# Kernel optimization log

Hardware: AMD Instinct MI355X
Metric: run time of the kernel (lower is better)

The kernel has to match this reference:

```python
import jax, jax.numpy as jnp
import numpy as np

J, C, F, K = 4096, 8192, 64, 2  # jobs, total nodes, out feats, TAGConv hops (DGL default K=2)


def setup_inputs() -> dict:
    key = jax.random.key(0)
    ks = jax.random.split(key, 8)
    h = jax.random.uniform(ks[0], (J,), jnp.float32)
    L = jax.random.uniform(ks[1], (J,), jnp.float32)
    W = jax.random.uniform(ks[2], (), jnp.float32)
    P = jax.random.uniform(ks[3], (), jnp.float32)
    N = jax.random.uniform(ks[4], (), jnp.float32)
    Graph = jax.random.randint(ks[5], (J, C), 0, 2).astype(jnp.float32)
    tag_w = jax.random.normal(ks[6], ((K + 1) * 6, F), jnp.float32) * 0.05  # TAGConv lin weight on concat of K+1 hops
    tag_b = jnp.zeros((F,), jnp.float32)
    lin_w = jax.random.normal(ks[7], (F, C), jnp.float32) * 0.05
    lin_b = jnp.zeros((C,), jnp.float32)
    return dict(h=h, L=L, W=W, P=P, N=N, Graph=Graph,
                tag_w=tag_w, tag_b=tag_b, lin_w=lin_w, lin_b=lin_b)


def _mask(Graph):
    Jn, Cn = Graph.shape
    row = Graph.sum(axis=1, keepdims=True)          # [J,1]
    col = Graph.sum(axis=0, keepdims=True)          # [1,C]
    colJ = col[:, :Jn]                               # [1,J]
    left = 1.0 - row - row.T - colJ - colJ.T         # [J,J]
    left = jnp.where(left == 1.0, 1.0, 0.0)
    left = jnp.triu(left, k=1)
    right = 1.0 - jnp.broadcast_to(row, (Jn, Cn - Jn))
    return jnp.concatenate([left, right], axis=1)    # [J,C]


def reference(h, L, W, P, N, Graph, tag_w, tag_b, lin_w, lin_b):
    Jn, Cn = Graph.shape
    # sort jobs by h descending, pair with L
    order = jnp.argsort(-h)
    jobList = jnp.stack([h[order], L[order]], axis=1)                 # [J,2]
    other = jnp.stack([W, P, N, jnp.asarray(1.0, h.dtype)])           # [4]
    X = jnp.concatenate([jobList, jnp.broadcast_to(other, (Jn, 4))], axis=1)  # [J,6]
    X = jnp.concatenate([X, jnp.zeros((Cn - Jn, 6), X.dtype)], axis=0)        # [C,6]
    # pad adjacency to square CxC
    A = jnp.concatenate([Graph, jnp.zeros((Cn - Jn, Cn), Graph.dtype)], axis=0)
    # DGL TAGConv: norm = clamp(in_deg,1)^-0.5; edge i->j iff A[i,j]==1 => aggregate = A^T @ x
    deg = A.sum(axis=0)
    norm = jnp.clip(deg, 1.0) ** -0.5

    def prop(x):
        return (A.T @ (x * norm[:, None])) * norm[:, None]

    f0 = X
    f1 = prop(f0)
    f2 = prop(f1)
    G_t = jnp.concatenate([f0, f1, f2], axis=1) @ tag_w + tag_b       # [C,F]
    Value = G_t[:Jn] @ lin_w + lin_b                                   # [J,C]
    tmp = Value - (1.0 - _mask(Graph)) * 10000.0
    Poss = jax.nn.softmax(tmp.reshape(-1)).reshape(tmp.shape)
    return (Value, Poss)
```

## Files before the change

kernel.cpp:

```cpp
#include <hip/hip_runtime.h>
#include <math.h>

#define JN 4096
#define CN 8192

typedef __attribute__((ext_vector_type(8))) short short8;
typedef __attribute__((ext_vector_type(4))) short short4v;
typedef __attribute__((ext_vector_type(4))) float f32x4;

#define WS_LWT    0
#define WS_GTB    262144
#define WS_ROWSUM 393216
#define WS_DEG    397312
#define WS_NORM   401408
#define WS_X      405504
#define WS_F1     430080
#define WS_PART   454656

#define PS_BITR    0
#define PS_P1      524288
#define PS_P2      917504

__device__ __forceinline__ unsigned short f2bf(float x) {
    unsigned int u = __float_as_uint(x);
    u += 0x7fffu + ((u >> 16) & 1u);
    return (unsigned short)(u >> 16);
}

__device__ __forceinline__ float gt_val(const float* __restrict__ x, const float* __restrict__ a,
                                        const float* __restrict__ b, const float* __restrict__ tw,
                                        float acc, int f) {
#pragma unroll
    for (int k = 0; k < 6; ++k) acc += x[k] * tw[k * 64 + f];
#pragma unroll
    for (int k = 0; k < 6; ++k) acc += a[k] * tw[(k + 6) * 64 + f];
#pragma unroll
    for (int k = 0; k < 6; ++k) acc += b[k] * tw[(k + 12) * 64 + f];
    return acc;
}

__global__ __launch_bounds__(256) void k_front(const float* __restrict__ G,
                                               const float* __restrict__ h, const float* __restrict__ L,
                                               const float* __restrict__ Wp, const float* __restrict__ Pp,
                                               const float* __restrict__ Np,
                                               const float* __restrict__ lw,
                                               float* __restrict__ rowsum,
                                               unsigned long long* __restrict__ bitR,
                                               float* __restrict__ X,
                                               unsigned short* __restrict__ lwT,
                                               float* __restrict__ deg) {
    __shared__ float redf[4];
    __shared__ int redi[4];
    __shared__ float s_t[64][65];
    int wv = threadIdx.x >> 6, lane = threadIdx.x & 63;
    if (blockIdx.x < JN) {
        int row = blockIdx.x;
        const f32x4* g4 = (const f32x4*)(G + (size_t)row * CN);
        unsigned long long* brow = bitR + (size_t)row * 64;
        float s = 0.f;
#pragma unroll
        for (int i = 0; i < 4; ++i) {
            f32x4 v = __builtin_nontemporal_load(&g4[i * 256 + wv * 64 + lane]);
            s += v[0] + v[1] + v[2] + v[3];
            unsigned long long b0 = __ballot(v[0] != 0.f);
            unsigned long long b1 = __ballot(v[1] != 0.f);
            unsigned long long b2 = __ballot(v[2] != 0.f);
            unsigned long long b3 = __ballot(v[3] != 0.f);
            if (!lane) {
                int base = i * 16 + wv * 4;
                brow[base] = b0; brow[base + 1] = b1; brow[base + 2] = b2; brow[base + 3] = b3;
            }
        }
#pragma unroll
        for (int i = 4; i < 8; ++i) {
            f32x4 v = __builtin_nontemporal_load(&g4[i * 256 + wv * 64 + lane]);
            s += v[0] + v[1] + v[2] + v[3];
        }
        for (int o = 32; o; o >>= 1) s += __shfl_down(s, o, 64);
        if (!lane) redf[wv] = s;
        __syncthreads();
        if (!threadIdx.x) rowsum[row] = redf[0] + redf[1] + redf[2] + redf[3];
    } else if (blockIdx.x < 2 * JN) {
        int i = blockIdx.x - JN;
        float hi = h[i];
        int cnt = 0;
        for (int j = threadIdx.x; j < JN; j += 256) {
            float hj = h[j];
            cnt += (hj > hi) || (hj == hi && j < i);
        }
        for (int o = 32; o; o >>= 1) cnt += __shfl_down(cnt, o, 64);
        if (!lane) redi[wv] = cnt;
        __syncthreads();
        if (!threadIdx.x) {
            int r = redi[0] + redi[1] + redi[2] + redi[3];
            float* xr = X + r * 6;
            xr[0] = hi; xr[1] = L[i]; xr[2] = *Wp; xr[3] = *Pp; xr[4] = *Np; xr[5] = 1.f;
        }
    } else if (blockIdx.x < 2 * JN + 128) {
        int c0 = (blockIdx.x - 2 * JN) * 64;
        for (int t = threadIdx.x; t < 4096; t += 256) {
            int f = t >> 6, cc = t & 63;
            s_t[f][cc] = lw[(size_t)f * CN + c0 + cc];
        }
        __syncthreads();
        for (int q = threadIdx.x; q < 512; q += 256) {
            int c = q >> 3, kc = q & 7;
            short8 pack;
#pragma unroll
            for (int i = 0; i < 8; ++i) pack[i] = (short)f2bf(s_t[kc * 8 + i][c]);
            *(short8*)(lwT + ((size_t)(c0 + c)) * 64 + kc * 8) = pack;
        }
    } else {
        for (int t = threadIdx.x; t < JN; t += 256) deg[t] = 0.f;
    }
}

__global__ __launch_bounds__(256) void k_colsum_bits(const unsigned long long* __restrict__ bitR,
                                                     float* __restrict__ deg) {
    __shared__ unsigned long long s_bits[256][4];
    int bx = blockIdx.x, r0 = blockIdx.y * 256;
    int tid = threadIdx.x;
    for (int t = tid; t < 1024; t += 256) {
        int r = t >> 2, wl = t & 3;
        s_bits[r][wl] = bitR[(size_t)(r0 + r) * 64 + bx * 4 + wl];
    }
    __syncthreads();
    int wl = tid & 3, bit = tid >> 2;
    int cnt = 0;
    for (int r = 0; r < 256; ++r)
        cnt += (int)((s_bits[r][wl] >> bit) & 1ull);
    atomicAdd(&deg[bx * 256 + tid], (float)cnt);
}

__global__ __launch_bounds__(256) void k_prop1(const unsigned long long* __restrict__ bitR,
                                               const float* __restrict__ X,
                                               const float* __restrict__ deg,
                                               float* __restrict__ norm,
                                               float* __restrict__ part) {
    __shared__ unsigned long long s_bits[256][4];
    __shared__ float s_in[1536];
    __shared__ float s_norm[256];
    int bx = blockIdx.x, r0 = blockIdx.y * 256;
    int tid = threadIdx.x;
    {
        float d = deg[r0 + tid];
        float dc = d < 1.f ? 1.f : d;
        float nv = rsqrtf(dc);
        s_norm[tid] = nv;
        if (bx == 0) norm[r0 + tid] = nv;
    }
    for (int t = tid; t < 1024; t += 256) {
        int r = t >> 2, wl = t & 3;
        s_bits[r][wl] = bitR[(size_t)(r0 + r) * 64 + bx * 4 + wl];
    }
    __syncthreads();
    for (int t = tid; t < 1536; t += 256)
        s_in[t] = X[r0 * 6 + t] * s_norm[t / 6];
    __syncthreads();
    int wl = tid & 3, bit = tid >> 2;
    float a0 = 0, a1 = 0, a2 = 0, a3 = 0, a4 = 0, a5 = 0;
    for (int r = 0; r < 256; ++r) {
        float g = (float)((s_bits[r][wl] >> bit) & 1ull);
        const float* x = &s_in[r * 6];
        a0 += g * x[0]; a1 += g * x[1]; a2 += g * x[2];
        a3 += g * x[3]; a4 += g * x[4]; a5 += g * x[5];
    }
    float* o = part + ((size_t)blockIdx.y * JN + bx * 256 + tid) * 6;
    o[0] = a0; o[1] = a1; o[2] = a2; o[3] = a3; o[4] = a4; o[5] = a5;
}

__global__ __launch_bounds__(256) void k_prop2(const unsigned long long* __restrict__ bitR,
                                               const float* __restrict__ p1, const float* __restrict__ norm,
                                               float* __restrict__ f1, float* __restrict__ part) {
    __shared__ unsigned long long s_bits[256][4];
    __shared__ float s_in[1536];
    int bx = blockIdx.x, r0 = blockIdx.y * 256;
    int tid = threadIdx.x;
    for (int t = tid; t < 1024; t += 256) {
        int r = t >> 2, wl = t & 3;
        s_bits[r][wl] = bitR[(size_t)(r0 + r) * 64 + bx * 4 + wl];
    }
    for (int t = tid; t < 1536; t += 256) {
        float s = 0.f;
        for (int ch = 0; ch < 16; ++ch) s += p1[(size_t)ch * 24576 + r0 * 6 + t];
        int row = r0 + t / 6;
        float n = norm[row];
        float f1v = s * n;
        if (bx == 0) f1[r0 * 6 + t] = f1v;
        s_in[t] = f1v * n;
    }
    __syncthreads();
    int wl = tid & 3, bit = tid >> 2;
    float a0 = 0, a1 = 0, a2 = 0, a3 = 0, a4 = 0, a5 = 0;
    for (int r = 0; r < 256; ++r) {
        float g = (float)((s_bits[r][wl] >> bit) & 1ull);
        const float* x = &s_in[r * 6];
        a0 += g * x[0]; a1 += g * x[1]; a2 += g * x[2];
        a3 += g * x[3]; a4 += g * x[4]; a5 += g * x[5];
    }
    float* o = part + ((size_t)blockIdx.y * JN + bx * 256 + tid) * 6;
    o[0] = a0; o[1] = a1; o[2] = a2; o[3] = a3; o[4] = a4; o[5] = a5;
}

__global__ __launch_bounds__(256) void k_gt(const float* __restrict__ p2, const float* __restrict__ norm,
                                            const float* __restrict__ f1, const float* __restrict__ X,
                                            const float* __restrict__ tw, const float* __restrict__ tb,
                                            unsigned short* __restrict__ Gtb) {
    __shared__ float s_x[64 * 6], s_f1[64 * 6], s_f2[64 * 6];
    __shared__ float s_tw[18 * 64], s_tb[64];
    int j0 = blockIdx.x * 64, tid = threadIdx.x;
    for (int t = tid; t < 1152; t += 256) s_tw[t] = tw[t];
    if (tid < 64) s_tb[tid] = tb[tid];
    for (int t = tid; t < 384; t += 256) {
        s_x[t] = X[j0 * 6 + t];
        s_f1[t] = f1[j0 * 6 + t];
        float s = 0.f;
        for (int ch = 0; ch < 16; ++ch) s += p2[(size_t)ch * 24576 + j0 * 6 + t];
        s_f2[t] = s * norm[j0 + t / 6];
    }
    __syncthreads();
    int row = tid & 63, fg = tid >> 6;
    float xv[6], av[6], bv[6];
#pragma unroll
    for (int k = 0; k < 6; ++k) {
        xv[k] = s_x[row * 6 + k]; av[k] = s_f1[row * 6 + k]; bv[k] = s_f2[row * 6 + k];
    }
    short8 p0, p1v;
#pragma unroll
    for (int i = 0; i < 16; ++i) {
        int f = fg * 16 + i;
        float acc = gt_val(xv, av, bv, s_tw, s_tb[f], f);
        unsigned short u = f2bf(acc);
        if (i < 8) p0[i] = (short)u; else p1v[i - 8] = (short)u;
    }
    *(short8*)(Gtb + (size_t)(j0 + row) * 64 + fg * 16) = p0;
    *(short8*)(Gtb + (size_t)(j0 + row) * 64 + fg * 16 + 8) = p1v;
}

#define GEMM_DECLS()                                                                      \
    __shared__ unsigned short sGt[64 * 64];                                               \
    __shared__ unsigned short sW[256 * 64];                                               \
    float* sRedM = (float*)sGt;                                                           \
    float* sRedS = ((float*)sGt) + 4;                                                     \
    float* sG    = ((float*)sGt) + 8;                                                     \
    (void)sRedM; (void)sRedS; (void)sG;

#define GEMM_BODY()                                                                       \
    int j0 = blockIdx.y * 64, c0 = blockIdx.x * 256, tid = threadIdx.x;                   \
    for (int q = tid; q < 2048; q += 256) {                                               \
        int col = q >> 3, off = q & 7;                                                    \
        short8 v = *(const short8*)(lwT + ((size_t)(c0 + col)) * 64 + off * 8);           \
        int byte = (col * 128 + off * 16) ^ ((col & 7) << 4);                             \
        *(short8*)((char*)sW + byte) = v;                                                 \
    }                                                                                     \
    for (int q = tid; q < 512; q += 256) {                                                \
        int row = q >> 3, off = q & 7;                                                    \
        short8 v = *(const short8*)(Gtb + ((size_t)(j0 + row)) * 64 + off * 8);           \
        int byte = (row * 128 + off * 16) ^ ((row & 7) << 4);                             \
        *(short8*)((char*)sGt + byte) = v;                                                \
    }                                                                                     \
    __syncthreads();                                                                      \
    int lane = tid & 63, w = tid >> 6;                                                    \
    int lrow = lane & 15, kg = lane >> 4;                                                 \
    f32x4 acc[4][4];                                            \
    for (int m = 0; m < 4; ++m)                                                           \
        for (int n = 0; n < 4; ++n) acc[m][n] = (f32x4){0.f, 0.f, 0.f, 0.f};              \
    for (int ks = 0; ks < 2; ++ks) {                                                      \
        int kb = ks * 64 + kg * 16;                                                       \
        short8 wf[4], gf[4];                                                              \
        for (int m = 0; m < 4; ++m) {                                                     \
            int col = w * 64 + m * 16 + lrow;                                             \
            wf[m] = *(const short8*)((const char*)sW + ((col * 128 + kb) ^ ((col & 7) << 4))); \
        }                                                                                 \
        for (int n = 0; n < 4; ++n) {                                                     \
            int row = n * 16 + lrow;                                                      \
            gf[n] = *(const short8*)((const char*)sGt + ((row * 128 + kb) ^ ((row & 7) << 4))); \
        }                                                                                 \
        for (int m = 0; m < 4; ++m)                                                       \
            for (int n = 0; n < 4; ++n)                                                   \
                acc[m][n] = __builtin_amdgcn_mfma_f32_16x16x32_bf16(wf[m], gf[n], acc[m][n], 0, 0, 0); \
    }                                                                                     \
    __syncthreads();                 \
    bool left = (c0 < JN);                                                                \
    int cb[4]; f32x4 lb4[4], rsc4[4], dgc4[4];                                            \
    for (int m = 0; m < 4; ++m) {                                                         \
        cb[m] = c0 + w * 64 + m * 16 + kg * 4;                                            \
        lb4[m] = *(const f32x4*)&lb[cb[m]];                                               \
        if (left) { rsc4[m] = *(const f32x4*)&rowsum[cb[m]]; dgc4[m] = *(const f32x4*)&deg[cb[m]]; } \
        else      { rsc4[m] = (f32x4){0,0,0,0}; dgc4[m] = (f32x4){0,0,0,0}; }             \
    }

__global__ __launch_bounds__(256) void k_valueA(const unsigned short* __restrict__ Gtb,
                                                const unsigned short* __restrict__ lwT,
                                                const float* __restrict__ lb,
                                                const float* __restrict__ rowsum, const float* __restrict__ deg,
                                                float* __restrict__ Value, float* __restrict__ partials) {
    GEMM_DECLS()
    GEMM_BODY()

    float mx = -INFINITY;
#pragma unroll
    for (int n = 0; n < 4; ++n) {
        int j = j0 + n * 16 + lrow;
        float rs_i = rowsum[j], dg_i = deg[j];
#pragma unroll
        for (int m = 0; m < 4; ++m) {
            f32x4 v4 = acc[m][n] + lb4[m];
            __builtin_nontemporal_store(v4, (f32x4*)&Value[(size_t)j * CN + cb[m]]);
            f32x4 t4;
#pragma unroll
            for (int u = 0; u < 4; ++u) {
                float om;
                if (left) {
                    bool m1 = ((rs_i + rsc4[m][u] + dg_i + dgc4[m][u]) == 0.0f) && (cb[m] + u > j);
                    om = m1 ? 0.f : 1.f;
                } else {
                    om = rs_i;
                }
                t4[u] = v4[u] - om * 10000.f;
            }
            acc[m][n] = t4;
            mx = fmaxf(fmaxf(fmaxf(mx, t4[0]), t4[1]), fmaxf(t4[2], t4[3]));
        }
    }
    float sm = 0.f;
#pragma unroll
    for (int n = 0; n < 4; ++n)
#pragma unroll
        for (int m = 0; m < 4; ++m)
#pragma unroll
            for (int u = 0; u < 4; ++u) sm += __expf(acc[m][n][u] - mx);

    for (int o = 32; o; o >>= 1) {
        float om_ = __shfl_down(mx, o, 64);
        float os_ = __shfl_down(sm, o, 64);
        float nm = fmaxf(mx, om_);
        sm = sm * __expf(mx - nm) + os_ * __expf(om_ - nm);
        mx = nm;
    }
    if (!lane) { sRedM[w] = mx; sRedS[w] = sm; }
    __syncthreads();
    if (!tid) {
        float M = sRedM[0], S = sRedS[0];
        for (int i = 1; i < 4; ++i) {
            float nm = fmaxf(M, sRedM[i]);
            S = S * __expf(M - nm) + sRedS[i] * __expf(sRedM[i] - nm);
            M = nm;
        }
        int bid = blockIdx.y * gridDim.x + blockIdx.x;
        partials[2 * bid] = M;
        partials[2 * bid + 1] = S;
    }
}

__global__ __launch_bounds__(256) void k_valueB(const unsigned short* __restrict__ Gtb,
                                                const unsigned short* __restrict__ lwT,
                                                const float* __restrict__ lb,
                                                const float* __restrict__ rowsum, const float* __restrict__ deg,
                                                const float* __restrict__ partials, float* __restrict__ Poss) {
    GEMM_DECLS()
    {
        int tid0 = threadIdx.x;
        float mx = -INFINITY, sm = 0.f;
        for (int i = tid0; i < 2048; i += 256) {
            float m = partials[2 * i], s = partials[2 * i + 1];
            float nm = fmaxf(mx, m);
            sm = sm * __expf(mx - nm) + s * __expf(m - nm);
            mx = nm;
        }
        for (int o = 32; o; o >>= 1) {
            float om_ = __shfl_down(mx, o, 64);
            float os_ = __shfl_down(sm, o, 64);
            float nm = fmaxf(mx, om_);
            sm = sm * __expf(mx - nm) + os_ * __expf(om_ - nm);
            mx = nm;
        }
        int lane0 = tid0 & 63, w0 = tid0 >> 6;
        if (!lane0) { sRedM[w0] = mx; sRedS[w0] = sm; }
        __syncthreads();
        if (!tid0) {
            float M = sRedM[0], S = sRedS[0];
            for (int i = 1; i < 4; ++i) {
                float nm = fmaxf(M, sRedM[i]);
                S = S * __expf(M - nm) + sRedS[i] * __expf(sRedM[i] - nm);
                M = nm;
            }
            sG[0] = M; sG[1] = S;
        }
        __syncthreads();
    }
    float gmax = sG[0];
    float ginv = 1.0f / sG[1];
    __syncthreads();

    GEMM_BODY()
#pragma unroll
    for (int n = 0; n < 4; ++n) {
        int j = j0 + n * 16 + lrow;
        float rs_i = rowsum[j], dg_i = deg[j];
#pragma unroll
        for (int m = 0; m < 4; ++m) {
            f32x4 v4 = acc[m][n] + lb4[m];
            f32x4 o4;
#pragma unroll
            for (int u = 0; u < 4; ++u) {
                float om;
                if (left) {
                    bool m1 = ((rs_i + rsc4[m][u] + dg_i + dgc4[m][u]) == 0.0f) && (cb[m] + u > j);
                    om = m1 ? 0.f : 1.f;
                } else {
                    om = rs_i;
                }
                o4[u] = __expf(v4[u] - om * 10000.f - gmax) * ginv;
            }
            __builtin_nontemporal_store(o4, (f32x4*)&Poss[(size_t)j * CN + cb[m]]);
        }
    }
}

extern "C" void kernel_launch(void* const* d_in, const int* in_sizes, int n_in,
                              void* d_out, int out_size, void* d_ws, size_t ws_size,
                              hipStream_t stream) {
    const float* h  = (const float*)d_in[0];
    const float* L  = (const float*)d_in[1];
    const float* W  = (const float*)d_in[2];
    const float* P  = (const float*)d_in[3];
    const float* N  = (const float*)d_in[4];
    const float* G  = (const float*)d_in[5];
    const float* tw = (const float*)d_in[6];
    const float* tb = (const float*)d_in[7];
    const float* lw = (const float*)d_in[8];
    const float* lb = (const float*)d_in[9];

    float* ws = (float*)d_ws;
    unsigned short* lwT = (unsigned short*)(ws + WS_LWT);
    unsigned short* Gtb = (unsigned short*)(ws + WS_GTB);
    float* rowsum = ws + WS_ROWSUM;
    float* deg    = ws + WS_DEG;
    float* norm   = ws + WS_NORM;
    float* X      = ws + WS_X;
    float* f1     = ws + WS_F1;
    float* part   = ws + WS_PART;

    float* Value = (float*)d_out;
    float* Poss  = Value + (size_t)JN * CN;

    unsigned long long* bitR = (unsigned long long*)(Poss + PS_BITR);
    float* p1      = Poss + PS_P1;
    float* p2      = Poss + PS_P2;

    k_front      <<<2 * JN + 129, 256, 0, stream>>>(G, h, L, W, P, N, lw, rowsum, bitR, X, lwT, deg);
    k_colsum_bits<<<dim3(16, 16), 256, 0, stream>>>(bitR, deg);
    k_prop1      <<<dim3(16, 16), 256, 0, stream>>>(bitR, X, deg, norm, p1);
    k_prop2      <<<dim3(16, 16), 256, 0, stream>>>(bitR, p1, norm, f1, p2);
    k_gt         <<<64, 256, 0, stream>>>(p2, norm, f1, X, tw, tb, Gtb);
    k_valueA     <<<dim3(32, 64), 256, 0, stream>>>(Gtb, lwT, lb, rowsum, deg, Value, part);
    k_valueB     <<<dim3(32, 64), 256, 0, stream>>>(Gtb, lwT, lb, rowsum, deg, part, Poss);
}
```

Measured before the change: 149.5 us.

## Fuse G_t computation into value GEMM kernels and merge front blocks

Removes the separate k_gt kernel: each value-GEMM block now recomputes its 64-row G_t tile from X, f1 and f2 straight into shared memory, and k_valueA saves f2 to workspace for k_valueB. The rank-sort work is also folded into the row-sum blocks of k_front, so its grid is halved. This saves one launch and a Gtb round trip through global memory. The cost is redundant G_t computation across the 32 column blocks, plus an extra 16-chunk p2 reduction in every k_valueA block.

```diff
diff --git a/kernel.cpp b/kernel.cpp
--- a/kernel.cpp
+++ b/kernel.cpp
@@ -5,11 +5,10 @@
 #define CN 8192
 
 typedef __attribute__((ext_vector_type(8))) short short8;
-typedef __attribute__((ext_vector_type(4))) short short4v;
 typedef __attribute__((ext_vector_type(4))) float f32x4;
 
 #define WS_LWT    0
-#define WS_GTB    262144
+#define WS_F2     262144
 #define WS_ROWSUM 393216
 #define WS_DEG    397312
 #define WS_NORM   401408
@@ -80,13 +79,12 @@
         if (!lane) redf[wv] = s;
         __syncthreads();
         if (!threadIdx.x) rowsum[row] = redf[0] + redf[1] + redf[2] + redf[3];
-    } else if (blockIdx.x < 2 * JN) {
-        int i = blockIdx.x - JN;
-        float hi = h[i];
+
+        float hi = h[row];
         int cnt = 0;
         for (int j = threadIdx.x; j < JN; j += 256) {
             float hj = h[j];
-            cnt += (hj > hi) || (hj == hi && j < i);
+            cnt += (hj > hi) || (hj == hi && j < row);
         }
         for (int o = 32; o; o >>= 1) cnt += __shfl_down(cnt, o, 64);
         if (!lane) redi[wv] = cnt;
@@ -94,10 +92,10 @@
         if (!threadIdx.x) {
             int r = redi[0] + redi[1] + redi[2] + redi[3];
             float* xr = X + r * 6;
-            xr[0] = hi; xr[1] = L[i]; xr[2] = *Wp; xr[3] = *Pp; xr[4] = *Np; xr[5] = 1.f;
-        }
-    } else if (blockIdx.x < 2 * JN + 128) {
-        int c0 = (blockIdx.x - 2 * JN) * 64;
+            xr[0] = hi; xr[1] = L[row]; xr[2] = *Wp; xr[3] = *Pp; xr[4] = *Np; xr[5] = 1.f;
+        }
+    } else if (blockIdx.x < JN + 128) {
+        int c0 = (blockIdx.x - JN) * 64;
         for (int t = threadIdx.x; t < 4096; t += 256) {
             int f = t >> 6, cc = t & 63;
             s_t[f][cc] = lw[(size_t)f * CN + c0 + cc];
@@ -202,62 +200,52 @@
     o[0] = a0; o[1] = a1; o[2] = a2; o[3] = a3; o[4] = a4; o[5] = a5;
 }
 
-__global__ __launch_bounds__(256) void k_gt(const float* __restrict__ p2, const float* __restrict__ norm,
-                                            const float* __restrict__ f1, const float* __restrict__ X,
-                                            const float* __restrict__ tw, const float* __restrict__ tb,
-                                            unsigned short* __restrict__ Gtb) {
-    __shared__ float s_x[64 * 6], s_f1[64 * 6], s_f2[64 * 6];
-    __shared__ float s_tw[18 * 64], s_tb[64];
-    int j0 = blockIdx.x * 64, tid = threadIdx.x;
-    for (int t = tid; t < 1152; t += 256) s_tw[t] = tw[t];
-    if (tid < 64) s_tb[tid] = tb[tid];
-    for (int t = tid; t < 384; t += 256) {
-        s_x[t] = X[j0 * 6 + t];
-        s_f1[t] = f1[j0 * 6 + t];
-        float s = 0.f;
-        for (int ch = 0; ch < 16; ++ch) s += p2[(size_t)ch * 24576 + j0 * 6 + t];
-        s_f2[t] = s * norm[j0 + t / 6];
-    }
-    __syncthreads();
-    int row = tid & 63, fg = tid >> 6;
-    float xv[6], av[6], bv[6];
-#pragma unroll
-    for (int k = 0; k < 6; ++k) {
-        xv[k] = s_x[row * 6 + k]; av[k] = s_f1[row * 6 + k]; bv[k] = s_f2[row * 6 + k];
-    }
-    short8 p0, p1v;
-#pragma unroll
-    for (int i = 0; i < 16; ++i) {
-        int f = fg * 16 + i;
-        float acc = gt_val(xv, av, bv, s_tw, s_tb[f], f);
-        unsigned short u = f2bf(acc);
-        if (i < 8) p0[i] = (short)u; else p1v[i - 8] = (short)u;
-    }
-    *(short8*)(Gtb + (size_t)(j0 + row) * 64 + fg * 16) = p0;
-    *(short8*)(Gtb + (size_t)(j0 + row) * 64 + fg * 16 + 8) = p1v;
-}
-
 #define GEMM_DECLS()                                                                      \
     __shared__ unsigned short sGt[64 * 64];                                               \
     __shared__ unsigned short sW[256 * 64];                                               \
     float* sRedM = (float*)sGt;                                                           \
     float* sRedS = ((float*)sGt) + 4;                                                     \
     float* sG    = ((float*)sGt) + 8;                                                     \
+    float* s_tw  = (float*)sW;                                                            \
+    float* s_tb  = ((float*)sW) + 1152;                                                   \
+    float* s_x   = ((float*)sW) + 1216;                                                   \
+    float* s_a   = ((float*)sW) + 1600;                                                   \
+    float* s_b   = ((float*)sW) + 1984;                                                   \
     (void)sRedM; (void)sRedS; (void)sG;
 
-#define GEMM_BODY()                                                                       \
+#define GEMM_BODY(F2_INIT)                                                                \
     int j0 = blockIdx.y * 64, c0 = blockIdx.x * 256, tid = threadIdx.x;                   \
-    for (int q = tid; q < 2048; q += 256) {                                               \
+    for (int t = tid; t < 1152; t += 256) s_tw[t] = tw[t];                                \
+    if (tid < 64) s_tb[tid] = tb[tid];                                                    \
+    for (int t = tid; t < 384; t += 256) {                                                \
+        s_x[t] = X[j0 * 6 + t];                                                           \
+        s_a[t] = f1[j0 * 6 + t];                                                          \
+        F2_INIT                                                                           \
+    }                                                                                     \
+    __syncthreads();                                                                      \
+    {       \
+        int row = tid & 63, fg = tid >> 6;                                                \
+        float xv[6], av[6], bv[6];                                                        \
+        for (int k = 0; k < 6; ++k) {                                                     \
+            xv[k] = s_x[row * 6 + k]; av[k] = s_a[row * 6 + k]; bv[k] = s_b[row * 6 + k]; \
+        }                                                                                 \
+        short8 pk0, pk1;                                                                  \
+        for (int i = 0; i < 16; ++i) {                                                    \
+            int f = fg * 16 + i;                                                          \
+            float acc = gt_val(xv, av, bv, s_tw, s_tb[f], f);                             \
+            unsigned short u = f2bf(acc);                                                 \
+            if (i < 8) pk0[i] = (short)u; else pk1[i - 8] = (short)u;                     \
+        }                                                                                 \
+        int base = row * 128 + fg * 32;                                                   \
+        *(short8*)((char*)sGt + (base ^ ((row & 7) << 4))) = pk0;                         \
+        *(short8*)((char*)sGt + ((base + 16) ^ ((row & 7) << 4))) = pk1;                  \
+    }                                                                                     \
+    __syncthreads();                                                                      \
+    for (int q = tid; q < 2048; q += 256) {              \
         int col = q >> 3, off = q & 7;                                                    \
         short8 v = *(const short8*)(lwT + ((size_t)(c0 + col)) * 64 + off * 8);           \
         int byte = (col * 128 + off * 16) ^ ((col & 7) << 4);                             \
         *(short8*)((char*)sW + byte) = v;                                                 \
-    }                                                                                     \
-    for (int q = tid; q < 512; q += 256) {                                                \
-        int row = q >> 3, off = q & 7;                                                    \
-        short8 v = *(const short8*)(Gtb + ((size_t)(j0 + row)) * 64 + off * 8);           \
-        int byte = (row * 128 + off * 16) ^ ((row & 7) << 4);                             \
-        *(short8*)((char*)sGt + byte) = v;                                                \
     }                                                                                     \
     __syncthreads();                                                                      \
     int lane = tid & 63, w = tid >> 6;                                                    \
@@ -290,13 +278,22 @@
         else      { rsc4[m] = (f32x4){0,0,0,0}; dgc4[m] = (f32x4){0,0,0,0}; }             \
     }
 
-__global__ __launch_bounds__(256) void k_valueA(const unsigned short* __restrict__ Gtb,
+__global__ __launch_bounds__(256) void k_valueA(const float* __restrict__ X, const float* __restrict__ f1,
+                                                const float* __restrict__ p2, const float* __restrict__ norm,
+                                                const float* __restrict__ tw, const float* __restrict__ tb,
                                                 const unsigned short* __restrict__ lwT,
                                                 const float* __restrict__ lb,
                                                 const float* __restrict__ rowsum, const float* __restrict__ deg,
+                                                float* __restrict__ f2ws,
                                                 float* __restrict__ Value, float* __restrict__ partials) {
     GEMM_DECLS()
-    GEMM_BODY()
+    GEMM_BODY({
+        float s = 0.f;
+        for (int ch = 0; ch < 16; ++ch) s += p2[(size_t)ch * 24576 + j0 * 6 + t];
+        float v = s * norm[j0 + t / 6];
+        s_b[t] = v;
+        if (blockIdx.x == 0) f2ws[j0 * 6 + t] = v;
+    })
 
     float mx = -INFINITY;
 #pragma unroll
@@ -353,7 +350,9 @@
     }
 }
 
-__global__ __launch_bounds__(256) void k_valueB(const unsigned short* __restrict__ Gtb,
+__global__ __launch_bounds__(256) void k_valueB(const float* __restrict__ X, const float* __restrict__ f1,
+                                                const float* __restrict__ f2ws,
+                                                const float* __restrict__ tw, const float* __restrict__ tb,
                                                 const unsigned short* __restrict__ lwT,
                                                 const float* __restrict__ lb,
                                                 const float* __restrict__ rowsum, const float* __restrict__ deg,
@@ -393,7 +392,9 @@
     float ginv = 1.0f / sG[1];
     __syncthreads();
 
-    GEMM_BODY()
+    GEMM_BODY({
+        s_b[t] = f2ws[j0 * 6 + t];
+    })
 #pragma unroll
     for (int n = 0; n < 4; ++n) {
         int j = j0 + n * 16 + lrow;
@@ -434,7 +435,7 @@
 
     float* ws = (float*)d_ws;
     unsigned short* lwT = (unsigned short*)(ws + WS_LWT);
-    unsigned short* Gtb = (unsigned short*)(ws + WS_GTB);
+    float* f2ws   = ws + WS_F2;
     float* rowsum = ws + WS_ROWSUM;
     float* deg    = ws + WS_DEG;
     float* norm   = ws + WS_NORM;
@@ -449,11 +450,10 @@
     float* p1      = Poss + PS_P1;
     float* p2      = Poss + PS_P2;
 
-    k_front      <<<2 * JN + 129, 256, 0, stream>>>(G, h, L, W, P, N, lw, rowsum, bitR, X, lwT, deg);
+    k_front      <<<JN + 129, 256, 0, stream>>>(G, h, L, W, P, N, lw, rowsum, bitR, X, lwT, deg);
     k_colsum_bits<<<dim3(16, 16), 256, 0, stream>>>(bitR, deg);
     k_prop1      <<<dim3(16, 16), 256, 0, stream>>>(bitR, X, deg, norm, p1);
     k_prop2      <<<dim3(16, 16), 256, 0, stream>>>(bitR, p1, norm, f1, p2);
-    k_gt         <<<64, 256, 0, stream>>>(p2, norm, f1, X, tw, tb, Gtb);
-    k_valueA     <<<dim3(32, 64), 256, 0, stream>>>(Gtb, lwT, lb, rowsum, deg, Value, part);
-    k_valueB     <<<dim3(32, 64), 256, 0, stream>>>(Gtb, lwT, lb, rowsum, deg, part, Poss);
-}
+    k_valueA     <<<dim3(32, 64), 256, 0, stream>>>(X, f1, p2, norm, tw, tb, lwT, lb, rowsum, deg, f2ws, Value, part);
+    k_valueB     <<<dim3(32, 64), 256, 0, stream>>>(X, f1, f2ws, tw, tb, lwT, lb, rowsum, deg, part, Poss);
+}
```

After: 163.9 us. +9.6%, slower.
